# Optimization experiments

Hardware: AMD Instinct MI355X
Metric: run time of the kernel (lower is better)

## Reference

```python
import jax, jax.numpy as jnp
import numpy as np

HEADS = 16
DIM_HEAD = 64

def setup_inputs() -> dict:
    key = jax.random.key(0)
    ks = jax.random.split(key, 7)
    B, Nq, Dq = 4, 2048, 1024
    Nk, Dc = 1024, 768
    inner = HEADS * DIM_HEAD  # 1024
    sq = 1.0 / np.sqrt(Dq)
    sc = 1.0 / np.sqrt(Dc)
    si = 1.0 / np.sqrt(inner)
    return {
        "x": jax.random.normal(ks[0], (B, Nq, Dq), dtype=jnp.float32),
        "context": jax.random.normal(ks[1], (B, Nk, Dc), dtype=jnp.float32),
        "Wq": jax.random.normal(ks[2], (Dq, inner), dtype=jnp.float32) * sq,
        "Wk": jax.random.normal(ks[3], (Dc, inner), dtype=jnp.float32) * sc,
        "Wv": jax.random.normal(ks[4], (Dc, inner), dtype=jnp.float32) * sc,
        "Wo": jax.random.normal(ks[5], (inner, Dq), dtype=jnp.float32) * si,
        "bo": jax.random.normal(ks[6], (Dq,), dtype=jnp.float32) * 0.01,
    }

def reference(x, context, Wq, Wk, Wv, Wo, bo):
    B, Nq, _ = x.shape
    Nk = context.shape[1]
    h, dh = HEADS, DIM_HEAD
    # projections (no bias on q/k/v, matching nn.Linear(bias=False))
    q = (x @ Wq).reshape(B, Nq, h, dh)        # [B,Nq,h,dh]
    k = (context @ Wk).reshape(B, Nk, h, dh)  # [B,Nk,h,dh]
    v = (context @ Wv).reshape(B, Nk, h, dh)
    scale = 1.0 / jnp.sqrt(jnp.asarray(dh, dtype=x.dtype))
    # scores: [B,h,Nq,Nk]
    scores = jnp.einsum('bqhd,bkhd->bhqk', q, k) * scale
    attn = jax.nn.softmax(scores, axis=-1)
    out = jnp.einsum('bhqk,bkhd->bqhd', attn, v).reshape(B, Nq, h * dh)
    return out @ Wo + bo
```

## Files before the change

kernel.cpp:

```cpp
#include <hip/hip_runtime.h>

typedef __bf16 bf16;
typedef __bf16 bf16x2 __attribute__((ext_vector_type(2)));
typedef __bf16 bf16x4 __attribute__((ext_vector_type(4)));
typedef __bf16 bf16x8 __attribute__((ext_vector_type(8)));
typedef float f32x4 __attribute__((ext_vector_type(4)));

#define MFMA(a, b, c) __builtin_amdgcn_mfma_f32_16x16x32_bf16(a, b, c, 0, 0, 0)

#define GLD16(gptr, ldsptr)                                                        \
  __builtin_amdgcn_global_load_lds(                                                \
      (const __attribute__((address_space(1))) unsigned int*)(gptr),               \
      (__attribute__((address_space(3))) unsigned int*)(ldsptr), 16, 0, 0)

union I4B8 { int4 i; bf16x8 v; };
union FI { float f; int i; };
union HI { bf16x2 h; int i; };

__global__ __launch_bounds__(256) void cast_k(const float* __restrict__ x,
                                              bf16* __restrict__ xb,
                                              const float* __restrict__ ctx,
                                              bf16* __restrict__ ctxb) {
  const int bid = blockIdx.x;
  const float* in;
  bf16* out;
  size_t i;
  if (bid < 4096) { in = x; out = xb; i = ((size_t)bid * 256 + threadIdx.x) * 8; }
  else { in = ctx; out = ctxb; i = ((size_t)(bid - 4096) * 256 + threadIdx.x) * 8; }
  const float4 a = *(const float4*)(in + i);
  const float4 b = *(const float4*)(in + i + 4);
  bf16x8 o;
  o[0] = (bf16)a.x; o[1] = (bf16)a.y; o[2] = (bf16)a.z; o[3] = (bf16)a.w;
  o[4] = (bf16)b.x; o[5] = (bf16)b.y; o[6] = (bf16)b.z; o[7] = (bf16)b.w;
  *(bf16x8*)(out + i) = o;
}

__global__ __launch_bounds__(256) void transpose_k(const float* __restrict__ Wq, bf16* __restrict__ WqT,
                                                   const float* __restrict__ Wk, bf16* __restrict__ WkvT,
                                                   const float* __restrict__ Wv,
                                                   const float* __restrict__ Wo, bf16* __restrict__ WoT) {
  __shared__ float t[32][33];
  const float* in; bf16* out; int R; float sc = 1.0f;
  const int z = blockIdx.z;
  if (z == 0)      { in = Wq; out = WqT;                R = 1024; sc = 0.18033688f; }
  else if (z == 1) { in = Wk; out = WkvT;               R = 768; }
  else if (z == 2) { in = Wv; out = WkvT + 1024 * 768;  R = 768; }
  else             { in = Wo; out = WoT;                R = 1024; }
  const int c0 = blockIdx.x * 32, r0 = blockIdx.y * 32;
  if (r0 >= R) return;
  const int tx = threadIdx.x & 31, ty = threadIdx.x >> 5;
#pragma unroll
  for (int i = 0; i < 4; i++)
    t[ty + i * 8][tx] = in[(size_t)(r0 + ty + i * 8) * 1024 + c0 + tx];
  __syncthreads();
#pragma unroll
  for (int i = 0; i < 4; i++)
    out[(size_t)(c0 + ty + i * 8) * R + r0 + tx] = (bf16)(t[tx][ty + i * 8] * sc);
}

template <int MODE>
__device__ __forceinline__ void gemm_body(const bf16* __restrict__ A,
                                          const bf16* __restrict__ Bt,
                                          int K, int m0, int n0,
                                          void* __restrict__ C0, void* __restrict__ C1,
                                          const float* __restrict__ bias,
                                          bf16* As, bf16* Bs) {
  const int tid = threadIdx.x;
  const int lane = tid & 63, wave = tid >> 6;
  const int wm = wave >> 1, wn = wave & 1;
  const int q = lane >> 4, c = lane & 15;

  f32x4 acc[4][4] = {};
  const bf16* Ag = A + (size_t)(m0 + (tid >> 2)) * K + (tid & 3) * 8;
  const bf16* Bg = Bt + (size_t)(n0 + (tid >> 2)) * K + (tid & 3) * 8;
  const size_t K64 = (size_t)K * 64;
  bf16* AsW = &As[wave * 512];
  bf16* BsW = &Bs[wave * 512];

  for (int k0 = 0; k0 < K; k0 += 32) {
    __syncthreads();
    GLD16(Ag + k0, AsW);
    GLD16(Ag + k0 + K64, AsW + 2048);
    GLD16(Bg + k0, BsW);
    GLD16(Bg + k0 + K64, BsW + 2048);
    __syncthreads();
    bf16x8 af[4], bfr[4];
#pragma unroll
    for (int mi = 0; mi < 4; mi++)
      af[mi] = *(const bf16x8*)&As[(wm * 64 + mi * 16 + c) * 32 + q * 8];
#pragma unroll
    for (int ni = 0; ni < 4; ni++)
      bfr[ni] = *(const bf16x8*)&Bs[(wn * 64 + ni * 16 + c) * 32 + q * 8];
#pragma unroll
    for (int mi = 0; mi < 4; mi++)
#pragma unroll
      for (int ni = 0; ni < 4; ni++) {
        if constexpr (MODE == 3)
          acc[mi][ni] = MFMA(af[mi], bfr[ni], acc[mi][ni]);
        else
          acc[mi][ni] = MFMA(bfr[ni], af[mi], acc[mi][ni]);
      }
  }

  if constexpr (MODE == 0 || MODE == 1) {
#pragma unroll
    for (int ni = 0; ni < 4; ni++) {
      const int col = n0 + wn * 64 + ni * 16 + q * 4;
      float4 bv4 = {};
      if constexpr (MODE == 1) bv4 = *(const float4*)&bias[col];
#pragma unroll
      for (int mi = 0; mi < 4; mi++) {
        const int row = m0 + wm * 64 + mi * 16 + c;
        if constexpr (MODE == 0) {
          bf16x4 vv;
#pragma unroll
          for (int r = 0; r < 4; r++) vv[r] = (bf16)acc[mi][ni][r];
          *(bf16x4*)&((bf16*)C0)[(size_t)row * 1024 + col] = vv;
        } else {
          f32x4 vv;
          vv[0] = acc[mi][ni][0] + bv4.x; vv[1] = acc[mi][ni][1] + bv4.y;
          vv[2] = acc[mi][ni][2] + bv4.z; vv[3] = acc[mi][ni][3] + bv4.w;
          *(f32x4*)&((float*)C0)[(size_t)row * 1024 + col] = vv;
        }
      }
    }
  } else {
#pragma unroll
    for (int ni = 0; ni < 4; ni++) {
      const int col = n0 + wn * 64 + ni * 16 + c;
#pragma unroll
      for (int mi = 0; mi < 4; mi++) {
        const int rbase = m0 + wm * 64 + mi * 16 + q * 4;
        const int b = rbase >> 10, key = rbase & 1023;
        if (col < 1024) {
          bf16* Kp = (bf16*)C0;
#pragma unroll
          for (int r = 0; r < 4; r++)
            Kp[(size_t)(rbase + r) * 1024 + col] = (bf16)acc[mi][ni][r];
        } else {
          bf16* VT = (bf16*)C1;
          const int h = (col - 1024) >> 6, d = (col - 1024) & 63;
          const int kl = key & 63;
          const int pkey = (key & ~63) | (kl & 32) | ((kl & 12) << 1) | ((kl & 16) >> 2);
          bf16x4 vv;
#pragma unroll
          for (int r = 0; r < 4; r++) vv[r] = (bf16)acc[mi][ni][r];
          *(bf16x4*)&VT[((size_t)(b * 16 + h) * 64 + d) * 1024 + pkey] = vv;
        }
      }
    }
  }
}

__global__ __launch_bounds__(256) void proj_k(const bf16* __restrict__ xb,
                                              const bf16* __restrict__ ctxb,
                                              const bf16* __restrict__ WqT,
                                              const bf16* __restrict__ WkvT,
                                              bf16* __restrict__ Q,
                                              bf16* __restrict__ Kp,
                                              bf16* __restrict__ VT) {
  __shared__ __align__(16) bf16 As[4096];
  __shared__ __align__(16) bf16 Bs[4096];
  const int bid = blockIdx.x;
  if (bid < 512) {
    gemm_body<0>(xb, WqT, 1024, (bid >> 3) * 128, (bid & 7) * 128, Q, nullptr, nullptr, As, Bs);
  } else {
    const int b2 = bid - 512;
    gemm_body<3>(ctxb, WkvT, 768, (b2 >> 4) * 128, (b2 & 15) * 128, Kp, VT, nullptr, As, Bs);
  }
}

__global__ __launch_bounds__(256) void out_k(const bf16* __restrict__ O,
                                             const bf16* __restrict__ WoT,
                                             float* __restrict__ out,
                                             const float* __restrict__ bo) {
  __shared__ __align__(16) bf16 As[4096];
  __shared__ __align__(16) bf16 Bs[4096];
  const int bid = blockIdx.x;
  gemm_body<1>(O, WoT, 1024, (bid >> 3) * 128, (bid & 7) * 128, out, nullptr, bo, As, Bs);
}

__global__ __launch_bounds__(256) void attn_k(const bf16* __restrict__ Qg,
                                              const bf16* __restrict__ Kg,
                                              const bf16* __restrict__ VTg,
                                              bf16* __restrict__ Og) {
  __shared__ __align__(16) bf16 Ks[64][72];
  __shared__ __align__(16) bf16 Vt[64][72];
  const int tid = threadIdx.x;
  const int lane = tid & 63, w = tid >> 6;
  const int q = lane >> 4, c = lane & 15;
  const int head = blockIdx.y, b = blockIdx.z;
  const int q0 = blockIdx.x * 128;

  bf16x8 aQ[2][2];
#pragma unroll
  for (int mj = 0; mj < 2; mj++)
#pragma unroll
    for (int ks = 0; ks < 2; ks++)
      aQ[mj][ks] = *(const bf16x8*)(Qg + (size_t)(b * 2048 + q0 + w * 32 + mj * 16 + c) * 1024 +
                                    head * 64 + ks * 32 + q * 8);

  f32x4 o[2][4] = {};
  float lsum[2] = {0.f, 0.f};

  const int srow = tid >> 2, sc = tid & 3;
  const bf16* Kbase = Kg + (size_t)(b * 1024 + srow) * 1024 + head * 64 + sc * 16;
  const bf16* Vbase = VTg + ((size_t)(b * 16 + head) * 64 + srow) * 1024 + sc * 16;

  for (int kt = 0; kt < 16; kt++) {
    const int key0 = kt * 64;
    __syncthreads();
    *(bf16x8*)&Ks[srow][sc * 16]     = *(const bf16x8*)(Kbase + (size_t)key0 * 1024);
    *(bf16x8*)&Ks[srow][sc * 16 + 8] = *(const bf16x8*)(Kbase + (size_t)key0 * 1024 + 8);
    *(bf16x8*)&Vt[srow][sc * 16]     = *(const bf16x8*)(Vbase + key0);
    *(bf16x8*)&Vt[srow][sc * 16 + 8] = *(const bf16x8*)(Vbase + key0 + 8);
    __syncthreads();

    f32x4 st[2][4] = {};
#pragma unroll
    for (int ks = 0; ks < 2; ks++) {
      bf16x8 ak[4];
#pragma unroll
      for (int ni = 0; ni < 4; ni++) ak[ni] = *(const bf16x8*)&Ks[ni * 16 + c][ks * 32 + q * 8];
#pragma unroll
      for (int mj = 0; mj < 2; mj++)
#pragma unroll
        for (int ni = 0; ni < 4; ni++)
          st[mj][ni] = MFMA(ak[ni], aQ[mj][ks], st[mj][ni]);
    }

    int pk[2][4][2];
#pragma unroll
    for (int mj = 0; mj < 2; mj++)
#pragma unroll
      for (int ni = 0; ni < 4; ni++) {
        float p0 = __builtin_amdgcn_exp2f(st[mj][ni][0]);
        float p1 = __builtin_amdgcn_exp2f(st[mj][ni][1]);
        float p2 = __builtin_amdgcn_exp2f(st[mj][ni][2]);
        float p3 = __builtin_amdgcn_exp2f(st[mj][ni][3]);
        lsum[mj] += (p0 + p1) + (p2 + p3);
        HI h0, h1;
        h0.h[0] = (bf16)p0; h0.h[1] = (bf16)p1;
        h1.h[0] = (bf16)p2; h1.h[1] = (bf16)p3;
        pk[mj][ni][0] = h0.i;
        pk[mj][ni][1] = h1.i;
      }

#pragma unroll
    for (int ks2 = 0; ks2 < 2; ks2++) {
      bf16x8 bv[4];
#pragma unroll
      for (int ni = 0; ni < 4; ni++)
        bv[ni] = *(const bf16x8*)&Vt[ni * 16 + c][ks2 * 32 + q * 8];
#pragma unroll
      for (int mi = 0; mi < 2; mi++) {
        I4B8 pa;
        pa.i.x = pk[mi][2 * ks2][0];
        pa.i.y = pk[mi][2 * ks2][1];
        pa.i.z = pk[mi][2 * ks2 + 1][0];
        pa.i.w = pk[mi][2 * ks2 + 1][1];
#pragma unroll
        for (int ni = 0; ni < 4; ni++)
          o[mi][ni] = MFMA(pa.v, bv[ni], o[mi][ni]);
      }
    }
  }

  FI rl[2];
#pragma unroll
  for (int mj = 0; mj < 2; mj++) {
    float l = lsum[mj];
    l += __shfl_xor(l, 16, 64);
    l += __shfl_xor(l, 32, 64);
    rl[mj].f = 1.0f / l;
  }

#pragma unroll
  for (int mi = 0; mi < 2; mi++) {
    FI rli[4];
#pragma unroll
    for (int r = 0; r < 4; r++)
      rli[r].i = __builtin_amdgcn_ds_bpermute((q * 4 + r) << 2, rl[mi].i);
#pragma unroll
    for (int ni = 0; ni < 4; ni++)
#pragma unroll
      for (int r = 0; r < 4; r++) {
        const int qrow = q0 + w * 32 + mi * 16 + q * 4 + r;
        const int col = head * 64 + ni * 16 + c;
        Og[(size_t)(b * 2048 + qrow) * 1024 + col] = (bf16)(o[mi][ni][r] * rli[r].f);
      }
  }
}

extern "C" void kernel_launch(void* const* d_in, const int* in_sizes, int n_in,
                              void* d_out, int out_size, void* d_ws, size_t ws_size,
                              hipStream_t stream) {
  (void)in_sizes; (void)n_in; (void)out_size; (void)ws_size;
  const float* x   = (const float*)d_in[0];
  const float* ctx = (const float*)d_in[1];
  const float* Wq  = (const float*)d_in[2];
  const float* Wk  = (const float*)d_in[3];
  const float* Wv  = (const float*)d_in[4];
  const float* Wo  = (const float*)d_in[5];
  const float* bo  = (const float*)d_in[6];
  float* out = (float*)d_out;

  char* ws = (char*)d_ws;
  const size_t MB = 1u << 20;
  bf16* WqT  = (bf16*)(ws);
  bf16* WkvT = (bf16*)(ws + 2 * MB);
  bf16* WoT  = (bf16*)(ws + 5 * MB);
  bf16* ctxb = (bf16*)(ws + 7 * MB);
  bf16* xb   = (bf16*)(ws + 13 * MB);
  bf16* Q    = (bf16*)(ws + 29 * MB);
  bf16* Kp   = (bf16*)(ws + 45 * MB);
  bf16* VT   = (bf16*)(ws + 53 * MB);
  bf16* O    = xb;

  cast_k<<<5632, 256, 0, stream>>>(x, xb, ctx, ctxb);
  transpose_k<<<dim3(32, 32, 4), 256, 0, stream>>>(Wq, WqT, Wk, WkvT, Wv, Wo, WoT);

  proj_k<<<1024, 256, 0, stream>>>(xb, ctxb, WqT, WkvT, Q, Kp, VT);

  attn_k<<<dim3(16, 16, 4), 256, 0, stream>>>(Q, Kp, VT, O);

  out_k<<<512, 256, 0, stream>>>(O, WoT, out, bo);
}
```

Before: 237.9 us.

## Merge prep kernels, split K/V projection, narrow out tile, prefetch K/V in attention

The cast and transpose launches are merged into one prep kernel to save a launch. The K and V projections become separate block ranges with simpler epilogues, removing the per-element branch. The output GEMM uses a 128x64 tile, doubling its block count so the grid fills the CUs better. The attention kernel prefetches the next K/V tile into registers while the current one is being computed, at the cost of extra register pressure.

New measurement: 237.0 us. Within noise of the previous version (-0.4%).

```diff
diff --git a/kernel.cpp b/kernel.cpp
--- a/kernel.cpp
+++ b/kernel.cpp
@@ -17,36 +17,34 @@
 union FI { float f; int i; };
 union HI { bf16x2 h; int i; };
 
-__global__ __launch_bounds__(256) void cast_k(const float* __restrict__ x,
-                                              bf16* __restrict__ xb,
-                                              const float* __restrict__ ctx,
-                                              bf16* __restrict__ ctxb) {
+__global__ __launch_bounds__(256) void prep_k(const float* __restrict__ x, bf16* __restrict__ xb,
+                                              const float* __restrict__ ctx, bf16* __restrict__ ctxb,
+                                              const float* __restrict__ Wq, bf16* __restrict__ WqT,
+                                              const float* __restrict__ Wk, bf16* __restrict__ WkvT,
+                                              const float* __restrict__ Wv,
+                                              const float* __restrict__ Wo, bf16* __restrict__ WoT) {
+  __shared__ float t[32][33];
   const int bid = blockIdx.x;
-  const float* in;
-  bf16* out;
-  size_t i;
-  if (bid < 4096) { in = x; out = xb; i = ((size_t)bid * 256 + threadIdx.x) * 8; }
-  else { in = ctx; out = ctxb; i = ((size_t)(bid - 4096) * 256 + threadIdx.x) * 8; }
-  const float4 a = *(const float4*)(in + i);
-  const float4 b = *(const float4*)(in + i + 4);
-  bf16x8 o;
-  o[0] = (bf16)a.x; o[1] = (bf16)a.y; o[2] = (bf16)a.z; o[3] = (bf16)a.w;
-  o[4] = (bf16)b.x; o[5] = (bf16)b.y; o[6] = (bf16)b.z; o[7] = (bf16)b.w;
-  *(bf16x8*)(out + i) = o;
-}
-
-__global__ __launch_bounds__(256) void transpose_k(const float* __restrict__ Wq, bf16* __restrict__ WqT,
-                                                   const float* __restrict__ Wk, bf16* __restrict__ WkvT,
-                                                   const float* __restrict__ Wv,
-                                                   const float* __restrict__ Wo, bf16* __restrict__ WoT) {
-  __shared__ float t[32][33];
+  if (bid < 5632) {
+    const float* in; bf16* out; size_t i;
+    if (bid < 4096) { in = x; out = xb; i = ((size_t)bid * 256 + threadIdx.x) * 8; }
+    else { in = ctx; out = ctxb; i = ((size_t)(bid - 4096) * 256 + threadIdx.x) * 8; }
+    const float4 a = *(const float4*)(in + i);
+    const float4 b = *(const float4*)(in + i + 4);
+    bf16x8 o;
+    o[0] = (bf16)a.x; o[1] = (bf16)a.y; o[2] = (bf16)a.z; o[3] = (bf16)a.w;
+    o[4] = (bf16)b.x; o[5] = (bf16)b.y; o[6] = (bf16)b.z; o[7] = (bf16)b.w;
+    *(bf16x8*)(out + i) = o;
+    return;
+  }
+  const int tt = bid - 5632;
+  const int z = tt >> 10, rem = tt & 1023;
   const float* in; bf16* out; int R; float sc = 1.0f;
-  const int z = blockIdx.z;
   if (z == 0)      { in = Wq; out = WqT;                R = 1024; sc = 0.18033688f; }
   else if (z == 1) { in = Wk; out = WkvT;               R = 768; }
   else if (z == 2) { in = Wv; out = WkvT + 1024 * 768;  R = 768; }
   else             { in = Wo; out = WoT;                R = 1024; }
-  const int c0 = blockIdx.x * 32, r0 = blockIdx.y * 32;
+  const int c0 = (rem & 31) * 32, r0 = (rem >> 5) * 32;
   if (r0 >= R) return;
   const int tx = threadIdx.x & 31, ty = threadIdx.x >> 5;
 #pragma unroll
@@ -58,19 +56,20 @@
     out[(size_t)(c0 + ty + i * 8) * R + r0 + tx] = (bf16)(t[tx][ty + i * 8] * sc);
 }
 
-template <int MODE>
+template <int MODE, int TN>
 __device__ __forceinline__ void gemm_body(const bf16* __restrict__ A,
                                           const bf16* __restrict__ Bt,
                                           int K, int m0, int n0,
-                                          void* __restrict__ C0, void* __restrict__ C1,
+                                          void* __restrict__ C0,
                                           const float* __restrict__ bias,
                                           bf16* As, bf16* Bs) {
+  constexpr int NI = TN / 32;
   const int tid = threadIdx.x;
   const int lane = tid & 63, wave = tid >> 6;
   const int wm = wave >> 1, wn = wave & 1;
   const int q = lane >> 4, c = lane & 15;
 
-  f32x4 acc[4][4] = {};
+  f32x4 acc[4][NI] = {};
   const bf16* Ag = A + (size_t)(m0 + (tid >> 2)) * K + (tid & 3) * 8;
   const bf16* Bg = Bt + (size_t)(n0 + (tid >> 2)) * K + (tid & 3) * 8;
   const size_t K64 = (size_t)K * 64;
@@ -82,20 +81,20 @@
     GLD16(Ag + k0, AsW);
     GLD16(Ag + k0 + K64, AsW + 2048);
     GLD16(Bg + k0, BsW);
-    GLD16(Bg + k0 + K64, BsW + 2048);
+    if constexpr (TN == 128) GLD16(Bg + k0 + K64, BsW + 2048);
     __syncthreads();
-    bf16x8 af[4], bfr[4];
+    bf16x8 af[4], bfr[NI];
 #pragma unroll
     for (int mi = 0; mi < 4; mi++)
       af[mi] = *(const bf16x8*)&As[(wm * 64 + mi * 16 + c) * 32 + q * 8];
 #pragma unroll
-    for (int ni = 0; ni < 4; ni++)
-      bfr[ni] = *(const bf16x8*)&Bs[(wn * 64 + ni * 16 + c) * 32 + q * 8];
+    for (int ni = 0; ni < NI; ni++)
+      bfr[ni] = *(const bf16x8*)&Bs[(wn * (TN / 2) + ni * 16 + c) * 32 + q * 8];
 #pragma unroll
     for (int mi = 0; mi < 4; mi++)
 #pragma unroll
-      for (int ni = 0; ni < 4; ni++) {
-        if constexpr (MODE == 3)
+      for (int ni = 0; ni < NI; ni++) {
+        if constexpr (MODE == 2)
           acc[mi][ni] = MFMA(af[mi], bfr[ni], acc[mi][ni]);
         else
           acc[mi][ni] = MFMA(bfr[ni], af[mi], acc[mi][ni]);
@@ -104,8 +103,8 @@
 
   if constexpr (MODE == 0 || MODE == 1) {
 #pragma unroll
-    for (int ni = 0; ni < 4; ni++) {
-      const int col = n0 + wn * 64 + ni * 16 + q * 4;
+    for (int ni = 0; ni < NI; ni++) {
+      const int col = n0 + wn * (TN / 2) + ni * 16 + q * 4;
       float4 bv4 = {};
       if constexpr (MODE == 1) bv4 = *(const float4*)&bias[col];
 #pragma unroll
@@ -126,27 +125,20 @@
     }
   } else {
 #pragma unroll
-    for (int ni = 0; ni < 4; ni++) {
-      const int col = n0 + wn * 64 + ni * 16 + c;
+    for (int ni = 0; ni < NI; ni++) {
+      const int col = n0 + wn * (TN / 2) + ni * 16 + c;
 #pragma unroll
       for (int mi = 0; mi < 4; mi++) {
         const int rbase = m0 + wm * 64 + mi * 16 + q * 4;
         const int b = rbase >> 10, key = rbase & 1023;
-        if (col < 1024) {
-          bf16* Kp = (bf16*)C0;
-#pragma unroll
-          for (int r = 0; r < 4; r++)
-            Kp[(size_t)(rbase + r) * 1024 + col] = (bf16)acc[mi][ni][r];
-        } else {
-          bf16* VT = (bf16*)C1;
-          const int h = (col - 1024) >> 6, d = (col - 1024) & 63;
-          const int kl = key & 63;
-          const int pkey = (key & ~63) | (kl & 32) | ((kl & 12) << 1) | ((kl & 16) >> 2);
-          bf16x4 vv;
-#pragma unroll
-          for (int r = 0; r < 4; r++) vv[r] = (bf16)acc[mi][ni][r];
-          *(bf16x4*)&VT[((size_t)(b * 16 + h) * 64 + d) * 1024 + pkey] = vv;
-        }
+        bf16* VT = (bf16*)C0;
+        const int h = col >> 6, d = col & 63;
+        const int kl = key & 63;
+        const int pkey = (key & ~63) | (kl & 32) | ((kl & 12) << 1) | ((kl & 16) >> 2);
+        bf16x4 vv;
+#pragma unroll
+        for (int r = 0; r < 4; r++) vv[r] = (bf16)acc[mi][ni][r];
+        *(bf16x4*)&VT[((size_t)(b * 16 + h) * 64 + d) * 1024 + pkey] = vv;
       }
     }
   }
@@ -163,10 +155,14 @@
   __shared__ __align__(16) bf16 Bs[4096];
   const int bid = blockIdx.x;
   if (bid < 512) {
-    gemm_body<0>(xb, WqT, 1024, (bid >> 3) * 128, (bid & 7) * 128, Q, nullptr, nullptr, As, Bs);
+    gemm_body<0, 128>(xb, WqT, 1024, (bid >> 3) * 128, (bid & 7) * 128, Q, nullptr, As, Bs);
+  } else if (bid < 768) {
+    const int b2 = bid - 512;
+    gemm_body<0, 128>(ctxb, WkvT, 768, (b2 >> 3) * 128, (b2 & 7) * 128, Kp, nullptr, As, Bs);
   } else {
-    const int b2 = bid - 512;
-    gemm_body<3>(ctxb, WkvT, 768, (b2 >> 4) * 128, (b2 & 15) * 128, Kp, VT, nullptr, As, Bs);
+    const int b3 = bid - 768;
+    gemm_body<2, 128>(ctxb, WkvT + (size_t)1024 * 768, 768, (b3 >> 3) * 128, (b3 & 7) * 128,
+                      VT, nullptr, As, Bs);
   }
 }
 
@@ -175,9 +171,9 @@
                                              float* __restrict__ out,
                                              const float* __restrict__ bo) {
   __shared__ __align__(16) bf16 As[4096];
-  __shared__ __align__(16) bf16 Bs[4096];
+  __shared__ __align__(16) bf16 Bs[2048];
   const int bid = blockIdx.x;
-  gemm_body<1>(O, WoT, 1024, (bid >> 3) * 128, (bid & 7) * 128, out, nullptr, bo, As, Bs);
+  gemm_body<1, 64>(O, WoT, 1024, (bid >> 4) * 128, (bid & 15) * 64, out, bo, As, Bs);
 }
 
 __global__ __launch_bounds__(256) void attn_k(const bf16* __restrict__ Qg,
@@ -207,13 +203,25 @@
   const bf16* Kbase = Kg + (size_t)(b * 1024 + srow) * 1024 + head * 64 + sc * 16;
   const bf16* Vbase = VTg + ((size_t)(b * 16 + head) * 64 + srow) * 1024 + sc * 16;
 
+  bf16x8 rk0 = *(const bf16x8*)(Kbase);
+  bf16x8 rk1 = *(const bf16x8*)(Kbase + 8);
+  bf16x8 rv0 = *(const bf16x8*)(Vbase);
+  bf16x8 rv1 = *(const bf16x8*)(Vbase + 8);
+
   for (int kt = 0; kt < 16; kt++) {
-    const int key0 = kt * 64;
     __syncthreads();
-    *(bf16x8*)&Ks[srow][sc * 16]     = *(const bf16x8*)(Kbase + (size_t)key0 * 1024);
-    *(bf16x8*)&Ks[srow][sc * 16 + 8] = *(const bf16x8*)(Kbase + (size_t)key0 * 1024 + 8);
-    *(bf16x8*)&Vt[srow][sc * 16]     = *(const bf16x8*)(Vbase + key0);
-    *(bf16x8*)&Vt[srow][sc * 16 + 8] = *(const bf16x8*)(Vbase + key0 + 8);
+    *(bf16x8*)&Ks[srow][sc * 16]     = rk0;
+    *(bf16x8*)&Ks[srow][sc * 16 + 8] = rk1;
+    *(bf16x8*)&Vt[srow][sc * 16]     = rv0;
+    *(bf16x8*)&Vt[srow][sc * 16 + 8] = rv1;
+    if (kt < 15) {
+      const size_t ko = (size_t)(kt + 1) * 64 * 1024;
+      const int vo = (kt + 1) * 64;
+      rk0 = *(const bf16x8*)(Kbase + ko);
+      rk1 = *(const bf16x8*)(Kbase + ko + 8);
+      rv0 = *(const bf16x8*)(Vbase + vo);
+      rv1 = *(const bf16x8*)(Vbase + vo + 8);
+    }
     __syncthreads();
 
     f32x4 st[2][4] = {};
@@ -317,12 +325,11 @@
   bf16* VT   = (bf16*)(ws + 53 * MB);
   bf16* O    = xb;
 
-  cast_k<<<5632, 256, 0, stream>>>(x, xb, ctx, ctxb);
-  transpose_k<<<dim3(32, 32, 4), 256, 0, stream>>>(Wq, WqT, Wk, WkvT, Wv, Wo, WoT);
+  prep_k<<<5632 + 4096, 256, 0, stream>>>(x, xb, ctx, ctxb, Wq, WqT, Wk, WkvT, Wv, Wo, WoT);
 
   proj_k<<<1024, 256, 0, stream>>>(xb, ctxb, WqT, WkvT, Q, Kp, VT);
 
   attn_k<<<dim3(16, 16, 4), 256, 0, stream>>>(Q, Kp, VT, O);
 
-  out_k<<<512, 256, 0, stream>>>(O, WoT, out, bo);
-}
+  out_k<<<1024, 256, 0, stream>>>(O, WoT, out, bo);
+}
```
